# Performance work log

Measured on AMD Instinct MI355X. Metric: run time of the kernel, lower is better.

## Reference

```python
import jax, jax.numpy as jnp
import numpy as np

N_CHANNELS = 1024
N_HEADS = 16
SEQ = 2048
BATCH = 2


def setup_inputs() -> dict:
    key = jax.random.key(0)
    k1, k2, k3 = jax.random.split(key, 3)
    x = jax.random.normal(k1, (BATCH, SEQ, N_CHANNELS), dtype=jnp.float32)
    qkv_w = jax.random.normal(k2, (3 * N_CHANNELS, N_CHANNELS), dtype=jnp.float32) * 0.02
    qkv_b = jnp.zeros((3 * N_CHANNELS,), dtype=jnp.float32)
    proj_w = jax.random.normal(k3, (N_CHANNELS, N_CHANNELS), dtype=jnp.float32) * 0.02
    proj_b = jnp.zeros((N_CHANNELS,), dtype=jnp.float32)
    return {"x": x, "qkv_w": qkv_w, "qkv_b": qkv_b, "proj_w": proj_w, "proj_b": proj_b}


def reference(x, qkv_w, qkv_b, proj_w, proj_b):
    bs, t, c = x.shape
    h = N_HEADS
    hd = c // h
    scale = hd ** (-0.5)
    # qkv projection: torch Linear is x @ W^T + b
    qkv = x @ qkv_w.T + qkv_b  # [B, T, 3C]
    qkv = qkv.reshape(bs, t, 3, h, hd)
    q, k, v = qkv[:, :, 0], qkv[:, :, 1], qkv[:, :, 2]  # each [B, T, H, hd]
    logits = jnp.einsum('bthc,bshc->bhts', q, k) * scale  # [B, H, T, T]
    # causal mask: log(tril(ones)) -> 0 below diag, -inf above
    causal = jnp.tril(jnp.ones((t, t), dtype=bool))
    logits = jnp.where(causal[None, None], logits, -jnp.inf)
    attn = jax.nn.softmax(logits, axis=-1)
    out = jnp.einsum('bhts,bshc->bthc', attn, v).reshape(bs, t, c)
    out = out @ proj_w.T + proj_b
    return out
```

## Files before the change

### kernel.cpp

```cpp
#include <hip/hip_runtime.h>

typedef __bf16 bf16x8 __attribute__((ext_vector_type(8)));
typedef float f32x4 __attribute__((ext_vector_type(4)));

__device__ inline ushort f2bf(float f) {
    unsigned u = __builtin_bit_cast(unsigned, f);
    unsigned r = (u + 0x7FFFu + ((u >> 16) & 1u)) >> 16;
    return (ushort)r;
}
__device__ inline float bf2f(ushort u) {
    unsigned x = ((unsigned)u) << 16;
    return __builtin_bit_cast(float, x);
}
__device__ inline uint4 pack8(const float* f) {
    uint4 r;
    r.x = (unsigned)f2bf(f[0]) | ((unsigned)f2bf(f[1]) << 16);
    r.y = (unsigned)f2bf(f[2]) | ((unsigned)f2bf(f[3]) << 16);
    r.z = (unsigned)f2bf(f[4]) | ((unsigned)f2bf(f[5]) << 16);
    r.w = (unsigned)f2bf(f[6]) | ((unsigned)f2bf(f[7]) << 16);
    return r;
}
__device__ inline unsigned cvtpk_bf16(float lo, float hi) {
    unsigned r;
    asm("v_cvt_pk_bf16_f32 %0, %1, %2" : "=v"(r) : "v"(lo), "v"(hi));
    return r;
}

#define MFMA_BF16(a, b, c) __builtin_amdgcn_mfma_f32_16x16x32_bf16(a, b, c, 0, 0, 0)
#define GLDS(g, l) __builtin_amdgcn_global_load_lds( \
    (const __attribute__((address_space(1))) void*)(g), \
    (__attribute__((address_space(3))) void*)(l), 16, 0, 0)

#define QSCALE 0.18033688011112042f

__global__ __launch_bounds__(256) void convert3(
    const float* __restrict__ s0, ushort* __restrict__ d0,
    const float* __restrict__ s1, ushort* __restrict__ d1,
    const float* __restrict__ s2, ushort* __restrict__ d2)
{
    const int i = blockIdx.x * 256 + threadIdx.x;
    const float* s; ushort* d; int off;
    if (i < 524288)      { s = s0; d = d0; off = i; }
    else if (i < 917504) { s = s1; d = d1; off = i - 524288; }
    else                 { s = s2; d = d2; off = i - 917504; }
    const float4* f = (const float4*)s + off * 2;
    float fa[8];
    *(float4*)&fa[0] = f[0];
    *(float4*)&fa[4] = f[1];
    ((uint4*)d)[off] = pack8(fa);
}

__global__ __launch_bounds__(256) void gemm_qkv(
    const ushort* __restrict__ A, const ushort* __restrict__ B,
    const float* __restrict__ bias,
    ushort* __restrict__ outQ, ushort* __restrict__ outK, ushort* __restrict__ outV,
    int N, int K)
{
    __shared__ __align__(16) ushort SMEM[32768];

    const int tid = threadIdx.x;
    const int w = tid >> 6;
    const int lane = tid & 63;
    const int l15 = lane & 15;
    const int quad = lane >> 4;
    const int srow = lane >> 3;

    const int bid = blockIdx.x + (blockIdx.y << 5);
    const int xcd = bid & 7;
    const int local = bid >> 3;
    const int mi_t = local & 7;
    const int ni_t = local >> 3;
    const int m0 = ((xcd & 3) * 8 + mi_t) * 128;
    const int n0 = (((xcd >> 2) * 12) + ni_t) * 128;
    const int wr = (w & 1) * 64;
    const int wc = (w >> 1) * 64;

    auto stage = [&](int k0, int buf) {
        ushort* As = SMEM + buf * 16384;
        ushort* Bs = As + 8192;
#pragma unroll
        for (int j = 0; j < 4; j++) {
            const int r0 = w * 32 + j * 8;
            const int row = r0 + srow;
            const int gcol = ((lane & 7) ^ (row & 7)) * 8;
            GLDS(A + (size_t)(m0 + row) * K + k0 + gcol, As + r0 * 64);
            GLDS(B + (size_t)(n0 + row) * K + k0 + gcol, Bs + r0 * 64);
        }
    };

    f32x4 acc[4][4] = {};

    stage(0, 0);
    __syncthreads();

    for (int k0 = 0; k0 < K; k0 += 64) {
        const int cur = (k0 >> 6) & 1;
        if (k0 + 64 < K) stage(k0 + 64, cur ^ 1);

        const ushort* As = SMEM + cur * 16384;
        const ushort* Bs = As + 8192;
        bf16x8 af[4][2], bf[4][2];
#pragma unroll
        for (int i = 0; i < 4; i++)
#pragma unroll
            for (int kk = 0; kk < 2; kk++) {
                const int ra = wr + i * 16 + l15;
                const int rb = wc + i * 16 + l15;
                af[i][kk] = *(const bf16x8*)&As[ra * 64 + (((kk * 4 + quad) ^ (ra & 7)) * 8)];
                bf[i][kk] = *(const bf16x8*)&Bs[rb * 64 + (((kk * 4 + quad) ^ (rb & 7)) * 8)];
            }
#pragma unroll
        for (int kk = 0; kk < 2; kk++)
#pragma unroll
            for (int mi = 0; mi < 4; mi++)
#pragma unroll
                for (int ni = 0; ni < 4; ni++)
                    acc[mi][ni] = MFMA_BF16(af[mi][kk], bf[ni][kk], acc[mi][ni]);
        __syncthreads();
    }

    const int which = n0 >> 10;
    ushort* Ct = SMEM;
    if (which == 2) {
#pragma unroll
        for (int mi = 0; mi < 4; mi++)
#pragma unroll
            for (int ni = 0; ni < 4; ni++)
#pragma unroll
                for (int r = 0; r < 4; r++) {
                    const int m_loc = wr + mi * 16 + quad * 4 + r;
                    const int n_loc = wc + ni * 16 + l15;
                    Ct[n_loc * 136 + m_loc] =
                        f2bf(acc[mi][ni][r] + bias[n0 + n_loc]);
                }
        __syncthreads();
        const int b = m0 >> 11;
#pragma unroll
        for (int i = 0; i < 8; i++) {
            const int vi = tid + i * 256;
            const int n_loc = vi >> 4, mblk = vi & 15;
            const uint4 val = *(const uint4*)&Ct[n_loc * 136 + mblk * 8];
            const int t = (m0 & 2047) + mblk * 8;
            const int c = (n0 + n_loc) & 1023;
            const int h = c >> 6, d = c & 63;
            *(uint4*)&outV[((size_t)(b * 16 + h) * 64 + d) * 2048 + t] = val;
        }
    } else {
        const float qs = (which == 0) ? QSCALE : 1.0f;
#pragma unroll
        for (int mi = 0; mi < 4; mi++)
#pragma unroll
            for (int ni = 0; ni < 4; ni++)
#pragma unroll
                for (int r = 0; r < 4; r++) {
                    const int m_loc = wr + mi * 16 + quad * 4 + r;
                    const int n_loc = wc + ni * 16 + l15;
                    Ct[m_loc * 136 + n_loc] =
                        f2bf((acc[mi][ni][r] + bias[n0 + n_loc]) * qs);
                }
        __syncthreads();
        ushort* outP = (which == 0) ? outQ : outK;
        const int hb = (n0 & 1023) >> 6;
        const int b = m0 >> 11;
#pragma unroll
        for (int i = 0; i < 8; i++) {
            const int vi = tid + i * 256;
            const int m_loc = vi >> 4, u = vi & 15;
            const uint4 val = *(const uint4*)&Ct[m_loc * 136 + u * 8];
            const int t = (m0 & 2047) + m_loc;
            const int h = hb + (u >> 3);
            const int d8 = (u & 7) * 8;
            *(uint4*)&outP[((size_t)(b * 16 + h)) * 131072 + (size_t)t * 64 + d8] = val;
        }
    }
}

__global__ __launch_bounds__(256) void gemm_proj(
    const ushort* __restrict__ A, const ushort* __restrict__ B,
    const float* __restrict__ bias, float* __restrict__ outD)
{
    const int N = 1024, K = 1024;
    __shared__ __align__(16) ushort SMEM[24576];

    const int tid = threadIdx.x;
    const int w = tid >> 6;
    const int lane = tid & 63;
    const int l15 = lane & 15;
    const int quad = lane >> 4;
    const int srow = lane >> 3;

    const int bid = blockIdx.x + (blockIdx.y << 6);
    const int nb = (bid & 7) * 64 + (bid >> 3);
    const int m0 = (nb >> 3) * 64;
    const int n0 = (nb & 7) * 128;
    const int wr = (w & 1) * 32;
    const int wc = (w >> 1) * 64;

    auto stage = [&](int k0, int buf) {
        ushort* As = SMEM + buf * 12288;
        ushort* Bs = As + 4096;
#pragma unroll
        for (int j = 0; j < 2; j++) {
            const int r0 = w * 16 + j * 8;
            const int row = r0 + srow;
            const int gcol = ((lane & 7) ^ (row & 7)) * 8;
            GLDS(A + (size_t)(m0 + row) * K + k0 + gcol, As + r0 * 64);
        }
#pragma unroll
        for (int j = 0; j < 4; j++) {
            const int r0 = w * 32 + j * 8;
            const int row = r0 + srow;
            const int gcol = ((lane & 7) ^ (row & 7)) * 8;
            GLDS(B + (size_t)(n0 + row) * K + k0 + gcol, Bs + r0 * 64);
        }
    };

    f32x4 acc[2][4] = {};

    stage(0, 0);
    __syncthreads();

    for (int k0 = 0; k0 < K; k0 += 64) {
        const int cur = (k0 >> 6) & 1;
        if (k0 + 64 < K) stage(k0 + 64, cur ^ 1);

        const ushort* As = SMEM + cur * 12288;
        const ushort* Bs = As + 4096;
        bf16x8 af[2][2], bf[4][2];
#pragma unroll
        for (int kk = 0; kk < 2; kk++) {
#pragma unroll
            for (int mi = 0; mi < 2; mi++) {
                const int ra = wr + mi * 16 + l15;
                af[mi][kk] = *(const bf16x8*)&As[ra * 64 + (((kk * 4 + quad) ^ (ra & 7)) * 8)];
            }
#pragma unroll
            for (int ni = 0; ni < 4; ni++) {
                const int rb = wc + ni * 16 + l15;
                bf[ni][kk] = *(const bf16x8*)&Bs[rb * 64 + (((kk * 4 + quad) ^ (rb & 7)) * 8)];
            }
        }
#pragma unroll
        for (int kk = 0; kk < 2; kk++)
#pragma unroll
            for (int mi = 0; mi < 2; mi++)
#pragma unroll
                for (int ni = 0; ni < 4; ni++)
                    acc[mi][ni] = MFMA_BF16(af[mi][kk], bf[ni][kk], acc[mi][ni]);
        __syncthreads();
    }

    float* Cf = (float*)SMEM;
#pragma unroll
    for (int cch = 0; cch < 2; cch++) {
        __syncthreads();
        if ((wc >> 6) == cch) {
#pragma unroll
            for (int mi = 0; mi < 2; mi++)
#pragma unroll
                for (int ni = 0; ni < 4; ni++)
#pragma unroll
                    for (int r = 0; r < 4; r++) {
                        const int m_loc = wr + mi * 16 + quad * 4 + r;
                        const int nl = ni * 16 + l15;
                        Cf[m_loc * 68 + nl] = acc[mi][ni][r] + bias[n0 + cch * 64 + nl];
                    }
        }
        __syncthreads();
#pragma unroll
        for (int i = 0; i < 4; i++) {
            const int vi = tid + i * 256;
            const int m_loc = vi >> 4, u = vi & 15;
            const float4 val = *(const float4*)&Cf[m_loc * 68 + u * 4];
            *(float4*)&outD[(size_t)(m0 + m_loc) * N + n0 + cch * 64 + u * 4] = val;
        }
    }
}

__global__ __launch_bounds__(256) void attn_split(
    const ushort* __restrict__ Q, const ushort* __restrict__ K,
    const ushort* __restrict__ Vt, ushort* __restrict__ O,
    ushort* __restrict__ Opart, float* __restrict__ Lpart)
{
    __shared__ __align__(16) ushort KV[2][2][64 * 64];

    const int bh = blockIdx.x;
    const int y = blockIdx.y;
    int qt, k0, k1, chunk, split;
    if (y < 48) {
        qt = 31 - (y >> 1); chunk = y & 1; split = 1;
        const int n = qt + 1, h = (n + 1) >> 1;
        k0 = chunk ? h : 0; k1 = chunk ? n : h;
    } else {
        qt = 55 - y; chunk = 0; split = 0; k0 = 0; k1 = qt + 1;
    }
    const int q0 = qt * 64;
    const int tid = threadIdx.x;
    const int w = tid >> 6;
    const int lane = tid & 63;
    const int l15 = lane & 15;
    const int quad = lane >> 4;

    auto stage = [&](int kt, int b) {
        const int t0 = kt * 64;
#pragma unroll
        for (int j = 0; j < 2; j++) {
            const int r0 = w * 16 + j * 8;
            const int row = r0 + (lane >> 3);
            const int gcol = ((lane & 7) ^ (row & 7)) * 8;
            GLDS(K + ((size_t)bh * 2048 + t0 + row) * 64 + gcol, &KV[b][0][r0 * 64]);
            GLDS(Vt + ((size_t)bh * 64 + row) * 2048 + t0 + gcol, &KV[b][1][r0 * 64]);
        }
    };

    const ushort* qbase = Q + ((size_t)bh * 2048 + q0 + w * 16 + l15) * 64;
    bf16x8 qf0 = *(const bf16x8*)(qbase + quad * 8);
    bf16x8 qf1 = *(const bf16x8*)(qbase + 32 + quad * 8);

    bf16x8 ones;
#pragma unroll
    for (int j = 0; j < 8; j++) ones[j] = (__bf16)1.0f;

    f32x4 oacc[4] = {};
    f32x4 lacc = {};

    const int qg = q0 + w * 16 + l15;

    stage(k0, 0);

    for (int kt = k0; kt < k1; kt++) {
        __syncthreads();
        if (kt + 1 < k1) stage(kt + 1, (kt + 1 - k0) & 1);

        const ushort* Ks = &KV[(kt - k0) & 1][0][0];
        const ushort* Vs = &KV[(kt - k0) & 1][1][0];
        const int t0 = kt * 64;

        f32x4 sacc[4] = {};
#pragma unroll
        for (int cb = 0; cb < 4; cb++) {
            const int rr = cb * 16 + l15;
            bf16x8 b0 = *(const bf16x8*)&Ks[rr * 64 + ((quad ^ (rr & 7)) * 8)];
            bf16x8 b1 = *(const bf16x8*)&Ks[rr * 64 + (((4 + quad) ^ (rr & 7)) * 8)];
            sacc[cb] = MFMA_BF16(b0, qf0, sacc[cb]);
            sacc[cb] = MFMA_BF16(b1, qf1, sacc[cb]);
        }

        unsigned pk[4][2];
        if (kt == qt) {
            const int kbase = t0 + quad * 4;
#pragma unroll
            for (int cb = 0; cb < 4; cb++) {
                float p[4];
#pragma unroll
                for (int r = 0; r < 4; r++) {
                    float x = sacc[cb][r];
                    if (kbase + cb * 16 + r > qg) x = -1e30f;
                    p[r] = __builtin_exp2f(x);
                }
                pk[cb][0] = cvtpk_bf16(p[0], p[1]);
                pk[cb][1] = cvtpk_bf16(p[2], p[3]);
            }
        } else {
#pragma unroll
            for (int cb = 0; cb < 4; cb++) {
                float p[4];
#pragma unroll
                for (int r = 0; r < 4; r++)
                    p[r] = __builtin_exp2f(sacc[cb][r]);
                pk[cb][0] = cvtpk_bf16(p[0], p[1]);
                pk[cb][1] = cvtpk_bf16(p[2], p[3]);
            }
        }

#pragma unroll
        for (int kc = 0; kc < 2; kc++) {
            unsigned x0 = pk[kc * 2][0], y0 = pk[kc * 2 + 1][0];
            unsigned x1 = pk[kc * 2][1], y1 = pk[kc * 2 + 1][1];
            asm("v_permlane32_swap_b32 %0, %1" : "+v"(x0), "+v"(y0));
            asm("v_permlane16_swap_b32 %0, %1" : "+v"(x0), "+v"(y0));
            asm("v_permlane32_swap_b32 %0, %1" : "+v"(x1), "+v"(y1));
            asm("v_permlane16_swap_b32 %0, %1" : "+v"(x1), "+v"(y1));
            uint4 av;
            av.x = x0; av.y = x1; av.z = y0; av.w = y1;
            bf16x8 af = __builtin_bit_cast(bf16x8, av);
#pragma unroll
            for (int cb = 0; cb < 4; cb++) {
                const int rr = cb * 16 + l15;
                bf16x8 bfr = *(const bf16x8*)&Vs[rr * 64 + (((kc * 4 + quad) ^ (rr & 7)) * 8)];
                oacc[cb] = MFMA_BF16(af, bfr, oacc[cb]);
            }
            lacc = MFMA_BF16(af, ones, lacc);
        }
    }

    if (!split) {
        const int b = bh >> 4, h = bh & 15;
#pragma unroll
        for (int r = 0; r < 4; r++) {
            const float inv = 1.0f / lacc[r];
            const int row = q0 + w * 16 + quad * 4 + r;
#pragma unroll
            for (int cb = 0; cb < 4; cb++) {
                const int col = h * 64 + cb * 16 + l15;
                O[((size_t)b * 2048 + row) * 1024 + col] = f2bf(oacc[cb][r] * inv);
            }
        }
    } else {
        const size_t slot2 = ((size_t)bh * 24 + (qt - 8)) * 2 + chunk;
        if (l15 == 0) {
#pragma unroll
            for (int r = 0; r < 4; r++)
                Lpart[slot2 * 64 + w * 16 + quad * 4 + r] = lacc[r];
        }
        __bf16* pw = (__bf16*)&KV[(k1 - k0) & 1][0][w * 1024];
        __builtin_amdgcn_wave_barrier();
#pragma unroll
        for (int cb = 0; cb < 4; cb++)
#pragma unroll
            for (int r = 0; r < 4; r++) {
                const int prow = quad * 4 + r;
                const int unit = cb * 2 + (l15 >> 3);
                pw[prow * 64 + ((unit ^ (prow & 7)) * 8) + (l15 & 7)] =
                    (__bf16)oacc[cb][r];
            }
        __builtin_amdgcn_s_waitcnt(0xC07F);
        __builtin_amdgcn_wave_barrier();
        const int r = lane >> 2, u = lane & 3;
        const int p0 = (2 * u) ^ (r & 7), p1 = (2 * u + 1) ^ (r & 7);
        const uint4 a = *(const uint4*)&pw[r * 64 + p0 * 8];
        const uint4 b = *(const uint4*)&pw[r * 64 + p1 * 8];
        ushort* dst = Opart + slot2 * 4096 + (w * 16 + r) * 64 + u * 16;
        *(uint4*)dst = a;
        *(uint4*)(dst + 8) = b;
    }
}

__global__ __launch_bounds__(256) void attn_combine(
    const ushort* __restrict__ Opart, const float* __restrict__ Lpart,
    ushort* __restrict__ O)
{
    const int bh = blockIdx.x;
    const int qt = 8 + blockIdx.y;
    const int tid = threadIdx.x;
    const int row = tid >> 2;
    const int cg = (tid & 3) * 16;
    const size_t s = ((size_t)bh * 24 + (qt - 8)) * 2;
    const ushort* p0 = Opart + s * 4096 + row * 64 + cg;
    const ushort* p1 = p0 + 4096;
    const float inv = 1.0f / (Lpart[s * 64 + row] + Lpart[(s + 1) * 64 + row]);
    const int b = bh >> 4, h = bh & 15;
    ushort* dst = O + ((size_t)b * 2048 + qt * 64 + row) * 1024 + h * 64 + cg;
    ushort out[16];
#pragma unroll
    for (int v = 0; v < 2; v++) {
        uint4 a = *(const uint4*)(p0 + v * 8);
        uint4 c = *(const uint4*)(p1 + v * 8);
        const ushort* ua = (const ushort*)&a;
        const ushort* uc = (const ushort*)&c;
#pragma unroll
        for (int j = 0; j < 8; j++)
            out[v * 8 + j] = f2bf((bf2f(ua[j]) + bf2f(uc[j])) * inv);
    }
    *(uint4*)dst = *(uint4*)&out[0];
    *(uint4*)(dst + 8) = *(uint4*)&out[8];
}

extern "C" void kernel_launch(void* const* d_in, const int* in_sizes, int n_in,
                              void* d_out, int out_size, void* d_ws, size_t ws_size,
                              hipStream_t stream) {
    const float* x      = (const float*)d_in[0];
    const float* qkv_w  = (const float*)d_in[1];
    const float* qkv_b  = (const float*)d_in[2];
    const float* proj_w = (const float*)d_in[3];
    const float* proj_b = (const float*)d_in[4];

    ushort* XbOb  = (ushort*)d_ws + 16;
    ushort* Wqkv  = XbOb + 4194304;
    ushort* Wproj = Wqkv + 3145728;
    ushort* Qb    = Wproj + 1048576;
    ushort* Kb    = Qb + 4194304;
    ushort* Vt    = Kb + 4194304;
    ushort* Opart = Vt + 4194304;
    float*  Lpart = (float*)(Opart + 6291456);

    convert3<<<4096, 256, 0, stream>>>(x, XbOb, qkv_w, Wqkv, proj_w, Wproj);
    gemm_qkv<<<dim3(32, 24), 256, 0, stream>>>(XbOb, Wqkv, qkv_b,
                                               Qb, Kb, Vt, 3072, 1024);
    attn_split<<<dim3(32, 56), 256, 0, stream>>>(Qb, Kb, Vt, XbOb, Opart, Lpart);
    attn_combine<<<dim3(32, 24), 256, 0, stream>>>(Opart, Lpart, XbOb);
    gemm_proj<<<dim3(64, 8), 256, 0, stream>>>(XbOb, Wproj, proj_b, (float*)d_out);
}
```

Baseline: 181.2 us.

## Split long causal attention rows into 2-4 KV chunks for better load balance

Attention query tiles are now split across more key chunks depending on their length: the longest quarter of tiles use 4 chunks, the next use 3, shorter ones use 2, and the first 8 stay unsplit. The grid grows from 56 to 80 tiles per head, and the combine kernel sums a variable number of partials. This is meant to shorten the critical path set by long causal rows and to fill more CUs. The partial buffers reuse the QKV weight scratch, which is dead after the QKV GEMM. The cost is more partial-output traffic and more combine work.

```diff
diff --git a/kernel.cpp b/kernel.cpp
--- a/kernel.cpp
+++ b/kernel.cpp
@@ -286,13 +286,26 @@
 
     const int bh = blockIdx.x;
     const int y = blockIdx.y;
-    int qt, k0, k1, chunk, split;
-    if (y < 48) {
-        qt = 31 - (y >> 1); chunk = y & 1; split = 1;
-        const int n = qt + 1, h = (n + 1) >> 1;
-        k0 = chunk ? h : 0; k1 = chunk ? n : h;
+    int qt, k0, k1, split, slot;
+    if (y < 32) {
+        qt = 31 - (y >> 2); const int ci = y & 3;
+        const int n = qt + 1;
+        k0 = ci * n / 4; k1 = (ci + 1) * n / 4;
+        split = 1; slot = 40 + (qt - 24) * 4 + ci;
+    } else if (y < 56) {
+        const int z = y - 32; const int t3 = z / 3;
+        qt = 23 - t3; const int ci = z - 3 * t3;
+        const int n = qt + 1;
+        k0 = ci * n / 3; k1 = (ci + 1) * n / 3;
+        split = 1; slot = 16 + (qt - 16) * 3 + ci;
+    } else if (y < 72) {
+        const int z = y - 56;
+        qt = 15 - (z >> 1); const int ci = z & 1;
+        const int n = qt + 1;
+        k0 = ci * n / 2; k1 = (ci + 1) * n / 2;
+        split = 1; slot = (qt - 8) * 2 + ci;
     } else {
-        qt = 55 - y; chunk = 0; split = 0; k0 = 0; k1 = qt + 1;
+        qt = 79 - y; split = 0; k0 = 0; k1 = qt + 1; slot = 0;
     }
     const int q0 = qt * 64;
     const int tid = threadIdx.x;
@@ -407,7 +420,7 @@
             }
         }
     } else {
-        const size_t slot2 = ((size_t)bh * 24 + (qt - 8)) * 2 + chunk;
+        const size_t slot2 = (size_t)bh * 72 + slot;
         if (l15 == 0) {
 #pragma unroll
             for (int r = 0; r < 4; r++)
@@ -442,28 +455,33 @@
 {
     const int bh = blockIdx.x;
     const int qt = 8 + blockIdx.y;
+    int c, base;
+    if (qt < 16)      { c = 2; base = (qt - 8) * 2; }
+    else if (qt < 24) { c = 3; base = 16 + (qt - 16) * 3; }
+    else              { c = 4; base = 40 + (qt - 24) * 4; }
     const int tid = threadIdx.x;
     const int row = tid >> 2;
     const int cg = (tid & 3) * 16;
-    const size_t s = ((size_t)bh * 24 + (qt - 8)) * 2;
-    const ushort* p0 = Opart + s * 4096 + row * 64 + cg;
-    const ushort* p1 = p0 + 4096;
-    const float inv = 1.0f / (Lpart[s * 64 + row] + Lpart[(s + 1) * 64 + row]);
+    const size_t s = (size_t)bh * 72 + base;
+    float lsum = 0.f;
+    for (int j = 0; j < c; j++) lsum += Lpart[(s + j) * 64 + row];
+    const float inv = 1.0f / lsum;
     const int b = bh >> 4, h = bh & 15;
     ushort* dst = O + ((size_t)b * 2048 + qt * 64 + row) * 1024 + h * 64 + cg;
-    ushort out[16];
 #pragma unroll
     for (int v = 0; v < 2; v++) {
-        uint4 a = *(const uint4*)(p0 + v * 8);
-        uint4 c = *(const uint4*)(p1 + v * 8);
-        const ushort* ua = (const ushort*)&a;
-        const ushort* uc = (const ushort*)&c;
-#pragma unroll
-        for (int j = 0; j < 8; j++)
-            out[v * 8 + j] = f2bf((bf2f(ua[j]) + bf2f(uc[j])) * inv);
-    }
-    *(uint4*)dst = *(uint4*)&out[0];
-    *(uint4*)(dst + 8) = *(uint4*)&out[8];
+        float accf[8] = {};
+        for (int j = 0; j < c; j++) {
+            uint4 a = *(const uint4*)(Opart + (s + j) * 4096 + row * 64 + cg + v * 8);
+            const ushort* ua = (const ushort*)&a;
+#pragma unroll
+            for (int t = 0; t < 8; t++) accf[t] += bf2f(ua[t]);
+        }
+        ushort out[8];
+#pragma unroll
+        for (int t = 0; t < 8; t++) out[t] = f2bf(accf[t] * inv);
+        *(uint4*)(dst + v * 8) = *(uint4*)out;
+    }
 }
 
 extern "C" void kernel_launch(void* const* d_in, const int* in_sizes, int n_in,
@@ -476,18 +494,18 @@
     const float* proj_b = (const float*)d_in[4];
 
     ushort* XbOb  = (ushort*)d_ws + 16;
-    ushort* Wqkv  = XbOb + 4194304;
-    ushort* Wproj = Wqkv + 3145728;
+    ushort* Wproj = XbOb + 4194304;
     ushort* Qb    = Wproj + 1048576;
     ushort* Kb    = Qb + 4194304;
     ushort* Vt    = Kb + 4194304;
-    ushort* Opart = Vt + 4194304;
-    float*  Lpart = (float*)(Opart + 6291456);
+    ushort* Wqkv  = Vt + 4194304;
+    ushort* Opart = Wqkv;
+    float*  Lpart = (float*)(Opart + 9437184);
 
     convert3<<<4096, 256, 0, stream>>>(x, XbOb, qkv_w, Wqkv, proj_w, Wproj);
     gemm_qkv<<<dim3(32, 24), 256, 0, stream>>>(XbOb, Wqkv, qkv_b,
                                                Qb, Kb, Vt, 3072, 1024);
-    attn_split<<<dim3(32, 56), 256, 0, stream>>>(Qb, Kb, Vt, XbOb, Opart, Lpart);
+    attn_split<<<dim3(32, 80), 256, 0, stream>>>(Qb, Kb, Vt, XbOb, Opart, Lpart);
     attn_combine<<<dim3(32, 24), 256, 0, stream>>>(Opart, Lpart, XbOb);
     gemm_proj<<<dim3(64, 8), 256, 0, stream>>>(XbOb, Wproj, proj_b, (float*)d_out);
 }
```

New measurement: 185.9 us, median of 2. 1.03x slower.
